# Optimization experiments

Measured on AMD Instinct MI355X. Metric: run time of the kernel, lower is better.

Reference implementation:

```python
import jax, jax.numpy as jnp
import numpy as np

N = 50000
E = 800000
NHID = 128
NOUT = 64
NLAYER = 4
BN_EPS = 1e-5


def setup_inputs() -> dict:
    key = jax.random.key(0)
    ks = jax.random.split(key, 4)
    x = jax.random.normal(ks[0], (N, NHID), dtype=jnp.float32)
    edge_index = jax.random.randint(ks[1], (2, E), 0, N, dtype=jnp.int32)
    Ws = jax.random.normal(ks[2], (NLAYER, NHID, NHID), dtype=jnp.float32) / np.sqrt(NHID)
    bs = jnp.zeros((NLAYER, NHID), dtype=jnp.float32)
    gammas = jnp.ones((NLAYER, NHID), dtype=jnp.float32)
    betas = jnp.zeros((NLAYER, NHID), dtype=jnp.float32)
    Wout = jax.random.normal(ks[3], (NHID, NOUT), dtype=jnp.float32) / np.sqrt(NHID)
    bout = jnp.zeros((NOUT,), dtype=jnp.float32)
    return {"x": x, "edge_index": edge_index, "Ws": Ws, "bs": bs,
            "gammas": gammas, "betas": betas, "Wout": Wout, "bout": bout}


def _gcn_conv(x, src, dst, norm, W, b):
    # GCNConv: h = x W, then symmetric-normalized scatter-add over edges (+ self loops already in src/dst)
    h = x @ W                                   # [N, nhid]
    msgs = h[src] * norm[:, None]               # [E+N, nhid] gather + scale
    agg = jax.ops.segment_sum(msgs, dst, num_segments=N)  # scatter-add
    return agg + b


def _batchnorm(x, gamma, beta):
    mean = jnp.mean(x, axis=0)
    var = jnp.mean(jnp.square(x - mean), axis=0)  # biased var (torch BN)
    return (x - mean) * jax.lax.rsqrt(var + BN_EPS) * gamma + beta


def reference(x, edge_index, Ws, bs, gammas, betas, Wout, bout):
    # add self loops
    loops = jnp.arange(N, dtype=edge_index.dtype)
    src = jnp.concatenate([edge_index[0], loops])
    dst = jnp.concatenate([edge_index[1], loops])
    # symmetric degree normalization: deg^-1/2[src] * deg^-1/2[dst]
    deg = jax.ops.segment_sum(jnp.ones_like(dst, dtype=x.dtype), dst, num_segments=N)
    dinv = jax.lax.rsqrt(jnp.maximum(deg, 1.0))
    norm = dinv[src] * dinv[dst]

    prev = x
    for l in range(NLAYER):
        h = _gcn_conv(x, src, dst, norm, Ws[l], bs[l])
        h = _batchnorm(h, gammas[l], betas[l])
        h = jax.nn.relu(h)
        # dropout p=0.0 -> identity
        x = h + prev  # residual
        prev = x
    return x @ Wout + bout
```

## Files before the change

### kernel.cpp

```cpp
#include <hip/hip_runtime.h>

#define NN 50000
#define NE 800000
#define NH 128
#define NO 64
#define NL 4
#define BN_EPS 1e-5f
#define NB1 ((NN + 255) / 256)

typedef __attribute__((ext_vector_type(8))) short short8;
typedef __attribute__((ext_vector_type(4))) float f32x4;

__device__ inline unsigned short f2bf(float f) {
    unsigned int u = __float_as_uint(f);
    return (unsigned short)((u + 0x7fffu + ((u >> 16) & 1u)) >> 16);
}
__device__ inline float bflo(unsigned int u) { return __uint_as_float(u << 16); }
__device__ inline float bfhi(unsigned int u) { return __uint_as_float(u & 0xffff0000u); }
__device__ inline unsigned pk(float a, float b) {
    return (unsigned)f2bf(a) | ((unsigned)f2bf(b) << 16);
}

__global__ void k_degrank(const int* __restrict__ dst, int* __restrict__ deg,
                          int* __restrict__ rank) {
    int base = (blockIdx.x * 256 + threadIdx.x) * 4;
    if (base >= NE) return;
    int4 d4 = *(const int4*)&dst[base];
    int4 r4;
    r4.x = atomicAdd(&deg[d4.x], 1);
    r4.y = atomicAdd(&deg[d4.y], 1);
    r4.z = atomicAdd(&deg[d4.z], 1);
    r4.w = atomicAdd(&deg[d4.w], 1);
    *(int4*)&rank[base] = r4;
}

__global__ void k_scan1(const int* __restrict__ deg, int* __restrict__ off,
                        int* __restrict__ aux, float* __restrict__ dinv) {
    __shared__ int ls[256];
    int i = blockIdx.x * 256 + threadIdx.x;
    int v = (i < NN) ? deg[i] : 0;
    ls[threadIdx.x] = v;
    __syncthreads();
    for (int s = 1; s < 256; s <<= 1) {
        int t = (threadIdx.x >= s) ? ls[threadIdx.x - s] : 0;
        __syncthreads();
        ls[threadIdx.x] += t;
        __syncthreads();
    }
    if (i < NN) {
        off[i] = ls[threadIdx.x] - v;
        dinv[i] = rsqrtf((float)v + 1.0f);
    }
    if (threadIdx.x == 255) aux[blockIdx.x] = ls[255];
}

__global__ void k_scan2(int* __restrict__ aux) {
    __shared__ int ls[256];
    int v = (threadIdx.x < NB1) ? aux[threadIdx.x] : 0;
    ls[threadIdx.x] = v;
    __syncthreads();
    for (int s = 1; s < 256; s <<= 1) {
        int t = (threadIdx.x >= s) ? ls[threadIdx.x - s] : 0;
        __syncthreads();
        ls[threadIdx.x] += t;
        __syncthreads();
    }
    if (threadIdx.x < NB1) aux[threadIdx.x] = ls[threadIdx.x] - v;
}

__global__ void k_scan3(int* __restrict__ off, const int* __restrict__ aux) {
    int i = blockIdx.x * 256 + threadIdx.x;
    if (i < NN) off[i] += aux[blockIdx.x];
}

__global__ void k_fill(const int* __restrict__ src, const int* __restrict__ dst,
                       const int* __restrict__ off, const int* __restrict__ rank,
                       int* __restrict__ csr) {
    int base = (blockIdx.x * 256 + threadIdx.x) * 4;
    if (base >= NE) return;
    int4 d4 = *(const int4*)&dst[base];
    int4 r4 = *(const int4*)&rank[base];
    int4 s4 = *(const int4*)&src[base];
    int o0 = off[d4.x], o1 = off[d4.y], o2 = off[d4.z], o3 = off[d4.w];
    csr[o0 + r4.x] = s4.x;
    csr[o1 + r4.y] = s4.y;
    csr[o2 + r4.z] = s4.z;
    csr[o3 + r4.w] = s4.w;
}

__global__ void k_pack(const float* __restrict__ Ws, const float* __restrict__ Wout,
                       unsigned short* __restrict__ Wpk, unsigned short* __restrict__ Wopk) {
    int t = blockIdx.x * 256 + threadIdx.x;
    if (t < NL * 16384) {
        int l = t >> 14, r = t & 16383;
        int ks = r >> 12, ct = (r >> 9) & 7, lane = (r >> 3) & 63, i = r & 7;
        int k = ks * 32 + (lane >> 4) * 8 + i;
        int n = ct * 16 + (lane & 15);
        Wpk[t] = f2bf(Ws[l * 16384 + k * 128 + n]);
    } else if (t < NL * 16384 + 8192) {
        int r = t - NL * 16384;
        int ks = r >> 11, ct = (r >> 9) & 3, lane = (r >> 3) & 63, i = r & 7;
        int k = ks * 32 + (lane >> 4) * 8 + i;
        int n = ct * 16 + (lane & 15);
        Wopk[r] = f2bf(Wout[k * 64 + n]);
    }
}

__global__ __launch_bounds__(256) void k_fg0(const float* __restrict__ X,
                                             const unsigned short* __restrict__ Wpk,
                                             const float* __restrict__ dinv,
                                             unsigned short* __restrict__ Hd) {
    int w = threadIdx.x >> 6, l = threadIdx.x & 63;
    int row0 = blockIdx.x * 64 + w * 16;
    int lo = l & 15, hi = l >> 4;
    int arow = row0 + lo;
    int crow = (arow < NN) ? arow : NN - 1;
    short8 frag[4];
#pragma unroll
    for (int g = 0; g < 4; g++) {
        int cs = g * 32 + hi * 8;
        float4 p0 = *(const float4*)&X[(size_t)crow * NH + cs];
        float4 p1 = *(const float4*)&X[(size_t)crow * NH + cs + 4];
        short8 f;
        f[0] = (short)f2bf(p0.x); f[1] = (short)f2bf(p0.y);
        f[2] = (short)f2bf(p0.z); f[3] = (short)f2bf(p0.w);
        f[4] = (short)f2bf(p1.x); f[5] = (short)f2bf(p1.y);
        f[6] = (short)f2bf(p1.z); f[7] = (short)f2bf(p1.w);
        frag[g] = f;
    }
    const short8* Wv = (const short8*)Wpk;
    int srow = row0 + hi * 4;
    float dv[4];
#pragma unroll
    for (int r = 0; r < 4; r++) dv[r] = (srow + r < NN) ? dinv[srow + r] : 0.0f;
#pragma unroll
    for (int ct = 0; ct < 8; ct++) {
        f32x4 acc = {0.0f, 0.0f, 0.0f, 0.0f};
#pragma unroll
        for (int g = 0; g < 4; g++)
            acc = __builtin_amdgcn_mfma_f32_16x16x32_bf16(frag[g], Wv[(g * 8 + ct) * 64 + l], acc, 0, 0, 0);
        int col = ct * 16 + lo;
#pragma unroll
        for (int r = 0; r < 4; r++) {
            int grow = srow + r;
            if (grow < NN) Hd[grow * NH + col] = f2bf(acc[r] * dv[r]);
        }
    }
}

__global__ __launch_bounds__(256) void k_fg(const unsigned short* __restrict__ AGGb,
                                            const float* __restrict__ scale,
                                            const float* __restrict__ shift,
                                            const float* __restrict__ Xprev,
                                            float* __restrict__ Xout,
                                            const unsigned short* __restrict__ Wpk,
                                            const float* __restrict__ dinv,
                                            unsigned short* __restrict__ Hd) {
    int w = threadIdx.x >> 6, l = threadIdx.x & 63;
    int row0 = blockIdx.x * 64 + w * 16;
    int lo = l & 15, hi = l >> 4;
    int arow = row0 + lo;
    bool valid = arow < NN;
    int crow = valid ? arow : NN - 1;
    short8 frag[4];
#pragma unroll
    for (int g = 0; g < 4; g++) {
        int cs = g * 32 + hi * 8;
        uint4 ab = *(const uint4*)&AGGb[(size_t)crow * NH + cs];
        float4 p0 = *(const float4*)&Xprev[(size_t)crow * NH + cs];
        float4 p1 = *(const float4*)&Xprev[(size_t)crow * NH + cs + 4];
        float4 sc0 = *(const float4*)&scale[cs];
        float4 sc1 = *(const float4*)&scale[cs + 4];
        float4 sh0 = *(const float4*)&shift[cs];
        float4 sh1 = *(const float4*)&shift[cs + 4];
        float o0 = fmaxf(fmaf(bflo(ab.x), sc0.x, sh0.x), 0.0f) + p0.x;
        float o1 = fmaxf(fmaf(bfhi(ab.x), sc0.y, sh0.y), 0.0f) + p0.y;
        float o2 = fmaxf(fmaf(bflo(ab.y), sc0.z, sh0.z), 0.0f) + p0.z;
        float o3 = fmaxf(fmaf(bfhi(ab.y), sc0.w, sh0.w), 0.0f) + p0.w;
        float o4 = fmaxf(fmaf(bflo(ab.z), sc1.x, sh1.x), 0.0f) + p1.x;
        float o5 = fmaxf(fmaf(bfhi(ab.z), sc1.y, sh1.y), 0.0f) + p1.y;
        float o6 = fmaxf(fmaf(bflo(ab.w), sc1.z, sh1.z), 0.0f) + p1.z;
        float o7 = fmaxf(fmaf(bfhi(ab.w), sc1.w, sh1.w), 0.0f) + p1.w;
        if (valid) {
            float4 s0 = {o0, o1, o2, o3}, s1 = {o4, o5, o6, o7};
            *(float4*)&Xout[(size_t)arow * NH + cs] = s0;
            *(float4*)&Xout[(size_t)arow * NH + cs + 4] = s1;
        }
        short8 f;
        f[0] = (short)f2bf(o0); f[1] = (short)f2bf(o1);
        f[2] = (short)f2bf(o2); f[3] = (short)f2bf(o3);
        f[4] = (short)f2bf(o4); f[5] = (short)f2bf(o5);
        f[6] = (short)f2bf(o6); f[7] = (short)f2bf(o7);
        frag[g] = f;
    }
    const short8* Wv = (const short8*)Wpk;
    int srow = row0 + hi * 4;
    float dv[4];
#pragma unroll
    for (int r = 0; r < 4; r++) dv[r] = (srow + r < NN) ? dinv[srow + r] : 0.0f;
#pragma unroll
    for (int ct = 0; ct < 8; ct++) {
        f32x4 acc = {0.0f, 0.0f, 0.0f, 0.0f};
#pragma unroll
        for (int g = 0; g < 4; g++)
            acc = __builtin_amdgcn_mfma_f32_16x16x32_bf16(frag[g], Wv[(g * 8 + ct) * 64 + l], acc, 0, 0, 0);
        int col = ct * 16 + lo;
#pragma unroll
        for (int r = 0; r < 4; r++) {
            int grow = srow + r;
            if (grow < NN) Hd[grow * NH + col] = f2bf(acc[r] * dv[r]);
        }
    }
}

__global__ __launch_bounds__(256) void k_fgout(const unsigned short* __restrict__ AGGb,
                                               const float* __restrict__ scale,
                                               const float* __restrict__ shift,
                                               const float* __restrict__ Xprev,
                                               const unsigned short* __restrict__ Wpk,
                                               const float* __restrict__ b,
                                               float* __restrict__ out) {
    int w = threadIdx.x >> 6, l = threadIdx.x & 63;
    int row0 = blockIdx.x * 64 + w * 16;
    int lo = l & 15, hi = l >> 4;
    int arow = row0 + lo;
    int crow = (arow < NN) ? arow : NN - 1;
    short8 frag[4];
#pragma unroll
    for (int g = 0; g < 4; g++) {
        int cs = g * 32 + hi * 8;
        uint4 ab = *(const uint4*)&AGGb[(size_t)crow * NH + cs];
        float4 p0 = *(const float4*)&Xprev[(size_t)crow * NH + cs];
        float4 p1 = *(const float4*)&Xprev[(size_t)crow * NH + cs + 4];
        float4 sc0 = *(const float4*)&scale[cs];
        float4 sc1 = *(const float4*)&scale[cs + 4];
        float4 sh0 = *(const float4*)&shift[cs];
        float4 sh1 = *(const float4*)&shift[cs + 4];
        short8 f;
        f[0] = (short)f2bf(fmaxf(fmaf(bflo(ab.x), sc0.x, sh0.x), 0.0f) + p0.x);
        f[1] = (short)f2bf(fmaxf(fmaf(bfhi(ab.x), sc0.y, sh0.y), 0.0f) + p0.y);
        f[2] = (short)f2bf(fmaxf(fmaf(bflo(ab.y), sc0.z, sh0.z), 0.0f) + p0.z);
        f[3] = (short)f2bf(fmaxf(fmaf(bfhi(ab.y), sc0.w, sh0.w), 0.0f) + p0.w);
        f[4] = (short)f2bf(fmaxf(fmaf(bflo(ab.z), sc1.x, sh1.x), 0.0f) + p1.x);
        f[5] = (short)f2bf(fmaxf(fmaf(bfhi(ab.z), sc1.y, sh1.y), 0.0f) + p1.y);
        f[6] = (short)f2bf(fmaxf(fmaf(bflo(ab.w), sc1.z, sh1.z), 0.0f) + p1.z);
        f[7] = (short)f2bf(fmaxf(fmaf(bfhi(ab.w), sc1.w, sh1.w), 0.0f) + p1.w);
        frag[g] = f;
    }
    const short8* Wv = (const short8*)Wpk;
    int srow = row0 + hi * 4;
#pragma unroll
    for (int ct = 0; ct < 4; ct++) {
        f32x4 acc = {0.0f, 0.0f, 0.0f, 0.0f};
#pragma unroll
        for (int g = 0; g < 4; g++)
            acc = __builtin_amdgcn_mfma_f32_16x16x32_bf16(frag[g], Wv[(g * 4 + ct) * 64 + l], acc, 0, 0, 0);
        int col = ct * 16 + lo;
        float bb = b[col];
#pragma unroll
        for (int r = 0; r < 4; r++) {
            int grow = srow + r;
            if (grow < NN) out[grow * NO + col] = acc[r] + bb;
        }
    }
}

__global__ __launch_bounds__(256) void k_gather(const unsigned short* __restrict__ Hd,
                                                const int* __restrict__ csr,
                                                const int* __restrict__ off,
                                                const int* __restrict__ deg,
                                                const float* __restrict__ dinv,
                                                unsigned short* __restrict__ AGGb) {
    int g = blockIdx.x * 16 + (threadIdx.x >> 4);
    if (g >= NN) return;
    int q = threadIdx.x & 15;
    const uint4* Hv = (const uint4*)Hd;
    int o = off[g], d = deg[g];
    uint4 h = Hv[g * 16 + q];
    float a0 = bflo(h.x), a1 = bfhi(h.x);
    float a2 = bflo(h.y), a3 = bfhi(h.y);
    float a4 = bflo(h.z), a5 = bfhi(h.z);
    float a6 = bflo(h.w), a7 = bfhi(h.w);
    int j = 0;
    for (; j + 4 <= d; j += 4) {
        int s0 = csr[o + j], s1 = csr[o + j + 1];
        int s2 = csr[o + j + 2], s3 = csr[o + j + 3];
        uint4 h0 = Hv[s0 * 16 + q];
        uint4 h1 = Hv[s1 * 16 + q];
        uint4 h2 = Hv[s2 * 16 + q];
        uint4 h3 = Hv[s3 * 16 + q];
        a0 += (bflo(h0.x) + bflo(h1.x)) + (bflo(h2.x) + bflo(h3.x));
        a1 += (bfhi(h0.x) + bfhi(h1.x)) + (bfhi(h2.x) + bfhi(h3.x));
        a2 += (bflo(h0.y) + bflo(h1.y)) + (bflo(h2.y) + bflo(h3.y));
        a3 += (bfhi(h0.y) + bfhi(h1.y)) + (bfhi(h2.y) + bfhi(h3.y));
        a4 += (bflo(h0.z) + bflo(h1.z)) + (bflo(h2.z) + bflo(h3.z));
        a5 += (bfhi(h0.z) + bfhi(h1.z)) + (bfhi(h2.z) + bfhi(h3.z));
        a6 += (bflo(h0.w) + bflo(h1.w)) + (bflo(h2.w) + bflo(h3.w));
        a7 += (bfhi(h0.w) + bfhi(h1.w)) + (bfhi(h2.w) + bfhi(h3.w));
    }
    for (; j < d; j++) {
        int s0 = csr[o + j];
        uint4 h0 = Hv[s0 * 16 + q];
        a0 += bflo(h0.x); a1 += bfhi(h0.x);
        a2 += bflo(h0.y); a3 += bfhi(h0.y);
        a4 += bflo(h0.z); a5 += bfhi(h0.z);
        a6 += bflo(h0.w); a7 += bfhi(h0.w);
    }
    float dv = dinv[g];
    uint4 u;
    u.x = pk(a0 * dv, a1 * dv);
    u.y = pk(a2 * dv, a3 * dv);
    u.z = pk(a4 * dv, a5 * dv);
    u.w = pk(a6 * dv, a7 * dv);
    ((uint4*)AGGb)[g * 16 + q] = u;
}

__global__ __launch_bounds__(256) void k_bn_stats(const unsigned short* __restrict__ AGGb,
                                                  float* __restrict__ sums,
                                                  float* __restrict__ sumsq) {
    int tid = threadIdx.x;
    int cq = tid & 31;
    int rg = tid >> 5;
    float s0 = 0, s1 = 0, s2 = 0, s3 = 0;
    float q0 = 0, q1 = 0, q2 = 0, q3 = 0;
    for (int r = blockIdx.x * 8 + rg; r < NN; r += gridDim.x * 8) {
        uint2 u = *(const uint2*)&AGGb[(size_t)r * NH + cq * 4];
        float v0 = bflo(u.x), v1 = bfhi(u.x), v2 = bflo(u.y), v3 = bfhi(u.y);
        s0 += v0; s1 += v1; s2 += v2; s3 += v3;
        q0 = fmaf(v0, v0, q0); q1 = fmaf(v1, v1, q1);
        q2 = fmaf(v2, v2, q2); q3 = fmaf(v3, v3, q3);
    }
    __shared__ float ls[256][4], lq[256][4];
    ls[tid][0] = s0; ls[tid][1] = s1; ls[tid][2] = s2; ls[tid][3] = s3;
    lq[tid][0] = q0; lq[tid][1] = q1; lq[tid][2] = q2; lq[tid][3] = q3;
    __syncthreads();
    if (rg == 0) {
        float t0 = s0, t1 = s1, t2 = s2, t3 = s3;
        float u0 = q0, u1 = q1, u2 = q2, u3 = q3;
        for (int g = 1; g < 8; g++) {
            t0 += ls[g * 32 + cq][0]; t1 += ls[g * 32 + cq][1];
            t2 += ls[g * 32 + cq][2]; t3 += ls[g * 32 + cq][3];
            u0 += lq[g * 32 + cq][0]; u1 += lq[g * 32 + cq][1];
            u2 += lq[g * 32 + cq][2]; u3 += lq[g * 32 + cq][3];
        }
        atomicAdd(&sums[cq * 4 + 0], t0); atomicAdd(&sums[cq * 4 + 1], t1);
        atomicAdd(&sums[cq * 4 + 2], t2); atomicAdd(&sums[cq * 4 + 3], t3);
        atomicAdd(&sumsq[cq * 4 + 0], u0); atomicAdd(&sumsq[cq * 4 + 1], u1);
        atomicAdd(&sumsq[cq * 4 + 2], u2); atomicAdd(&sumsq[cq * 4 + 3], u3);
    }
}

__global__ void k_bn_fin(const float* __restrict__ sums, const float* __restrict__ sumsq,
                         const float* __restrict__ gamma, const float* __restrict__ beta,
                         float* __restrict__ scale, float* __restrict__ shift) {
    int c = threadIdx.x;
    if (c < NH) {
        float mean = sums[c] * (1.0f / NN);
        float var = sumsq[c] * (1.0f / NN) - mean * mean;
        float istd = rsqrtf(var + BN_EPS);
        float sc = istd * gamma[c];
        scale[c] = sc;
        shift[c] = beta[c] - mean * sc;
    }
}

extern "C" void kernel_launch(void* const* d_in, const int* in_sizes, int n_in,
                              void* d_out, int out_size, void* d_ws, size_t ws_size,
                              hipStream_t stream) {
    const float* x    = (const float*)d_in[0];
    const int*   ei   = (const int*)d_in[1];
    const float* Ws   = (const float*)d_in[2];
    const float* gam  = (const float*)d_in[4];
    const float* bet  = (const float*)d_in[5];
    const float* Wout = (const float*)d_in[6];
    const float* bout = (const float*)d_in[7];
    float* out = (float*)d_out;

    const int* src = ei;
    const int* dst = ei + NE;

    char* p = (char*)d_ws;
    auto alloc = [&](size_t bytes) { char* r = p; p += (bytes + 255) & ~(size_t)255; return r; };
    int*   deg_i = (int*)alloc(NN * 4);
    int*   off   = (int*)alloc(NN * 4);
    int*   rank  = (int*)alloc((size_t)NE * 4);
    int*   aux   = (int*)alloc(256 * 4);
    int*   csr   = (int*)alloc((size_t)NE * 4);
    float* dinv  = (float*)alloc(NN * 4);
    float* XA    = (float*)alloc((size_t)NN * NH * 4);
    float* XB    = (float*)alloc((size_t)NN * NH * 4);
    unsigned short* Hd   = (unsigned short*)alloc((size_t)NN * NH * 2);
    unsigned short* AGGb = (unsigned short*)alloc((size_t)NN * NH * 2);
    unsigned short* Wpk  = (unsigned short*)alloc((size_t)NL * NH * NH * 2);
    unsigned short* Wopk = (unsigned short*)alloc((size_t)NH * NO * 2);
    float* stats = (float*)alloc(NL * 2 * NH * 4);
    float* scale = (float*)alloc(NH * 4);
    float* shift = (float*)alloc(NH * 4);

    hipMemsetAsync(deg_i, 0, NN * 4, stream);
    hipMemsetAsync(stats, 0, NL * 2 * NH * 4, stream);
    k_degrank<<<(NE / 4 + 255) / 256, 256, 0, stream>>>(dst, deg_i, rank);
    k_scan1<<<NB1, 256, 0, stream>>>(deg_i, off, aux, dinv);
    k_scan2<<<1, 256, 0, stream>>>(aux);
    k_scan3<<<NB1, 256, 0, stream>>>(off, aux);
    k_fill<<<(NE / 4 + 255) / 256, 256, 0, stream>>>(src, dst, off, rank, csr);
    k_pack<<<(NL * 16384 + 8192 + 255) / 256, 256, 0, stream>>>(Ws, Wout, Wpk, Wopk);

    const int GB = (NN + 63) / 64;

    k_fg0<<<GB, 256, 0, stream>>>(x, Wpk, dinv, Hd);

    const float* xprev = x;
    for (int l = 0; l < NL; l++) {
        float* sums  = stats + (size_t)l * 2 * NH;
        float* sumsq = sums + NH;
        k_gather<<<(NN + 15) / 16, 256, 0, stream>>>(Hd, csr, off, deg_i, dinv, AGGb);
        k_bn_stats<<<128, 256, 0, stream>>>(AGGb, sums, sumsq);
        k_bn_fin<<<1, 128, 0, stream>>>(sums, sumsq, gam + l * NH, bet + l * NH, scale, shift);
        if (l < NL - 1) {
            float* Xout = (l & 1) ? XB : XA;
            k_fg<<<GB, 256, 0, stream>>>(AGGb, scale, shift, xprev, Xout,
                                         Wpk + (size_t)(l + 1) * 16384, dinv, Hd);
            xprev = Xout;
        } else {
            k_fgout<<<GB, 256, 0, stream>>>(AGGb, scale, shift, xprev, Wopk, bout, out);
        }
    }
}
```

Baseline: 385.8 us.

## Fuse BN statistics into gather via per-block partials, drop scan3 kernel

The gather kernel now computes per-block column sums and sums of squares of the aggregated rows with shuffles and shared memory. It writes them to a partials buffer, and a new 128-block reduction kernel turns them into BN scale and shift. This removes the separate stats pass over AGGb, the float atomics, the finalize kernel and the stats memset. The scan3 kernel is also removed by adding the block offset from aux at each use. Degree counting now handles two edges per thread instead of four. The stats are taken from the fp32 values before bf16 rounding, which changes numerics slightly, and every gather block now pays for an extra reduction.

```diff
diff --git a/kernel.cpp b/kernel.cpp
--- a/kernel.cpp
+++ b/kernel.cpp
@@ -7,6 +7,7 @@
 #define NL 4
 #define BN_EPS 1e-5f
 #define NB1 ((NN + 255) / 256)
+#define NGB (NN / 16)
 
 typedef __attribute__((ext_vector_type(8))) short short8;
 typedef __attribute__((ext_vector_type(4))) float f32x4;
@@ -23,15 +24,13 @@
 
 __global__ void k_degrank(const int* __restrict__ dst, int* __restrict__ deg,
                           int* __restrict__ rank) {
-    int base = (blockIdx.x * 256 + threadIdx.x) * 4;
+    int base = (blockIdx.x * 256 + threadIdx.x) * 2;
     if (base >= NE) return;
-    int4 d4 = *(const int4*)&dst[base];
-    int4 r4;
-    r4.x = atomicAdd(&deg[d4.x], 1);
-    r4.y = atomicAdd(&deg[d4.y], 1);
-    r4.z = atomicAdd(&deg[d4.z], 1);
-    r4.w = atomicAdd(&deg[d4.w], 1);
-    *(int4*)&rank[base] = r4;
+    int2 d2 = *(const int2*)&dst[base];
+    int2 r2;
+    r2.x = atomicAdd(&deg[d2.x], 1);
+    r2.y = atomicAdd(&deg[d2.y], 1);
+    *(int2*)&rank[base] = r2;
 }
 
 __global__ void k_scan1(const int* __restrict__ deg, int* __restrict__ off,
@@ -68,24 +67,18 @@
     if (threadIdx.x < NB1) aux[threadIdx.x] = ls[threadIdx.x] - v;
 }
 
-__global__ void k_scan3(int* __restrict__ off, const int* __restrict__ aux) {
-    int i = blockIdx.x * 256 + threadIdx.x;
-    if (i < NN) off[i] += aux[blockIdx.x];
-}
-
 __global__ void k_fill(const int* __restrict__ src, const int* __restrict__ dst,
-                       const int* __restrict__ off, const int* __restrict__ rank,
-                       int* __restrict__ csr) {
+                       const int* __restrict__ off, const int* __restrict__ aux,
+                       const int* __restrict__ rank, int* __restrict__ csr) {
     int base = (blockIdx.x * 256 + threadIdx.x) * 4;
     if (base >= NE) return;
     int4 d4 = *(const int4*)&dst[base];
     int4 r4 = *(const int4*)&rank[base];
     int4 s4 = *(const int4*)&src[base];
-    int o0 = off[d4.x], o1 = off[d4.y], o2 = off[d4.z], o3 = off[d4.w];
-    csr[o0 + r4.x] = s4.x;
-    csr[o1 + r4.y] = s4.y;
-    csr[o2 + r4.z] = s4.z;
-    csr[o3 + r4.w] = s4.w;
+    csr[off[d4.x] + aux[d4.x >> 8] + r4.x] = s4.x;
+    csr[off[d4.y] + aux[d4.y >> 8] + r4.y] = s4.y;
+    csr[off[d4.z] + aux[d4.z >> 8] + r4.z] = s4.z;
+    csr[off[d4.w] + aux[d4.w >> 8] + r4.w] = s4.w;
 }
 
 __global__ void k_pack(const float* __restrict__ Ws, const float* __restrict__ Wout,
@@ -268,99 +261,114 @@
 __global__ __launch_bounds__(256) void k_gather(const unsigned short* __restrict__ Hd,
                                                 const int* __restrict__ csr,
                                                 const int* __restrict__ off,
+                                                const int* __restrict__ aux,
                                                 const int* __restrict__ deg,
                                                 const float* __restrict__ dinv,
-                                                unsigned short* __restrict__ AGGb) {
-    int g = blockIdx.x * 16 + (threadIdx.x >> 4);
-    if (g >= NN) return;
-    int q = threadIdx.x & 15;
-    const uint4* Hv = (const uint4*)Hd;
-    int o = off[g], d = deg[g];
-    uint4 h = Hv[g * 16 + q];
-    float a0 = bflo(h.x), a1 = bfhi(h.x);
-    float a2 = bflo(h.y), a3 = bfhi(h.y);
-    float a4 = bflo(h.z), a5 = bfhi(h.z);
-    float a6 = bflo(h.w), a7 = bfhi(h.w);
-    int j = 0;
-    for (; j + 4 <= d; j += 4) {
-        int s0 = csr[o + j], s1 = csr[o + j + 1];
-        int s2 = csr[o + j + 2], s3 = csr[o + j + 3];
-        uint4 h0 = Hv[s0 * 16 + q];
-        uint4 h1 = Hv[s1 * 16 + q];
-        uint4 h2 = Hv[s2 * 16 + q];
-        uint4 h3 = Hv[s3 * 16 + q];
-        a0 += (bflo(h0.x) + bflo(h1.x)) + (bflo(h2.x) + bflo(h3.x));
-        a1 += (bfhi(h0.x) + bfhi(h1.x)) + (bfhi(h2.x) + bfhi(h3.x));
-        a2 += (bflo(h0.y) + bflo(h1.y)) + (bflo(h2.y) + bflo(h3.y));
-        a3 += (bfhi(h0.y) + bfhi(h1.y)) + (bfhi(h2.y) + bfhi(h3.y));
-        a4 += (bflo(h0.z) + bflo(h1.z)) + (bflo(h2.z) + bflo(h3.z));
-        a5 += (bfhi(h0.z) + bfhi(h1.z)) + (bfhi(h2.z) + bfhi(h3.z));
-        a6 += (bflo(h0.w) + bflo(h1.w)) + (bflo(h2.w) + bflo(h3.w));
-        a7 += (bfhi(h0.w) + bfhi(h1.w)) + (bfhi(h2.w) + bfhi(h3.w));
-    }
-    for (; j < d; j++) {
-        int s0 = csr[o + j];
-        uint4 h0 = Hv[s0 * 16 + q];
-        a0 += bflo(h0.x); a1 += bfhi(h0.x);
-        a2 += bflo(h0.y); a3 += bfhi(h0.y);
-        a4 += bflo(h0.z); a5 += bfhi(h0.z);
-        a6 += bflo(h0.w); a7 += bfhi(h0.w);
-    }
-    float dv = dinv[g];
-    uint4 u;
-    u.x = pk(a0 * dv, a1 * dv);
-    u.y = pk(a2 * dv, a3 * dv);
-    u.z = pk(a4 * dv, a5 * dv);
-    u.w = pk(a6 * dv, a7 * dv);
-    ((uint4*)AGGb)[g * 16 + q] = u;
-}
-
-__global__ __launch_bounds__(256) void k_bn_stats(const unsigned short* __restrict__ AGGb,
-                                                  float* __restrict__ sums,
-                                                  float* __restrict__ sumsq) {
-    int tid = threadIdx.x;
-    int cq = tid & 31;
-    int rg = tid >> 5;
-    float s0 = 0, s1 = 0, s2 = 0, s3 = 0;
-    float q0 = 0, q1 = 0, q2 = 0, q3 = 0;
-    for (int r = blockIdx.x * 8 + rg; r < NN; r += gridDim.x * 8) {
-        uint2 u = *(const uint2*)&AGGb[(size_t)r * NH + cq * 4];
-        float v0 = bflo(u.x), v1 = bfhi(u.x), v2 = bflo(u.y), v3 = bfhi(u.y);
-        s0 += v0; s1 += v1; s2 += v2; s3 += v3;
-        q0 = fmaf(v0, v0, q0); q1 = fmaf(v1, v1, q1);
-        q2 = fmaf(v2, v2, q2); q3 = fmaf(v3, v3, q3);
-    }
-    __shared__ float ls[256][4], lq[256][4];
-    ls[tid][0] = s0; ls[tid][1] = s1; ls[tid][2] = s2; ls[tid][3] = s3;
-    lq[tid][0] = q0; lq[tid][1] = q1; lq[tid][2] = q2; lq[tid][3] = q3;
+                                                unsigned short* __restrict__ AGGb,
+                                                float* __restrict__ partial) {
+    int b = blockIdx.x;
+    int slot = threadIdx.x >> 4, q = threadIdx.x & 15;
+    int g = b * 16 + slot;
+    float a0 = 0, a1 = 0, a2 = 0, a3 = 0, a4 = 0, a5 = 0, a6 = 0, a7 = 0;
+    if (g < NN) {
+        const uint4* Hv = (const uint4*)Hd;
+        int o = off[g] + aux[g >> 8];
+        int d = deg[g];
+        uint4 h = Hv[g * 16 + q];
+        a0 = bflo(h.x); a1 = bfhi(h.x);
+        a2 = bflo(h.y); a3 = bfhi(h.y);
+        a4 = bflo(h.z); a5 = bfhi(h.z);
+        a6 = bflo(h.w); a7 = bfhi(h.w);
+        int j = 0;
+        for (; j + 4 <= d; j += 4) {
+            int s0 = csr[o + j], s1 = csr[o + j + 1];
+            int s2 = csr[o + j + 2], s3 = csr[o + j + 3];
+            uint4 h0 = Hv[s0 * 16 + q];
+            uint4 h1 = Hv[s1 * 16 + q];
+            uint4 h2 = Hv[s2 * 16 + q];
+            uint4 h3 = Hv[s3 * 16 + q];
+            a0 += (bflo(h0.x) + bflo(h1.x)) + (bflo(h2.x) + bflo(h3.x));
+            a1 += (bfhi(h0.x) + bfhi(h1.x)) + (bfhi(h2.x) + bfhi(h3.x));
+            a2 += (bflo(h0.y) + bflo(h1.y)) + (bflo(h2.y) + bflo(h3.y));
+            a3 += (bfhi(h0.y) + bfhi(h1.y)) + (bfhi(h2.y) + bfhi(h3.y));
+            a4 += (bflo(h0.z) + bflo(h1.z)) + (bflo(h2.z) + bflo(h3.z));
+            a5 += (bfhi(h0.z) + bfhi(h1.z)) + (bfhi(h2.z) + bfhi(h3.z));
+            a6 += (bflo(h0.w) + bflo(h1.w)) + (bflo(h2.w) + bflo(h3.w));
+            a7 += (bfhi(h0.w) + bfhi(h1.w)) + (bfhi(h2.w) + bfhi(h3.w));
+        }
+        for (; j < d; j++) {
+            int s0 = csr[o + j];
+            uint4 h0 = Hv[s0 * 16 + q];
+            a0 += bflo(h0.x); a1 += bfhi(h0.x);
+            a2 += bflo(h0.y); a3 += bfhi(h0.y);
+            a4 += bflo(h0.z); a5 += bfhi(h0.z);
+            a6 += bflo(h0.w); a7 += bfhi(h0.w);
+        }
+        float dv = dinv[g];
+        a0 *= dv; a1 *= dv; a2 *= dv; a3 *= dv;
+        a4 *= dv; a5 *= dv; a6 *= dv; a7 *= dv;
+        uint4 u;
+        u.x = pk(a0, a1); u.y = pk(a2, a3);
+        u.z = pk(a4, a5); u.w = pk(a6, a7);
+        ((uint4*)AGGb)[g * 16 + q] = u;
+    }
+    float t0 = a0 * a0, t1 = a1 * a1, t2 = a2 * a2, t3 = a3 * a3;
+    float t4 = a4 * a4, t5 = a5 * a5, t6 = a6 * a6, t7 = a7 * a7;
+#define RED(v) v += __shfl_xor(v, 16); v += __shfl_xor(v, 32);
+    RED(a0) RED(a1) RED(a2) RED(a3) RED(a4) RED(a5) RED(a6) RED(a7)
+    RED(t0) RED(t1) RED(t2) RED(t3) RED(t4) RED(t5) RED(t6) RED(t7)
+#undef RED
+    __shared__ float ws[4][16][16];
+    int wv = threadIdx.x >> 6, lane = threadIdx.x & 63;
+    if (lane < 16) {
+        ws[wv][lane][0] = a0; ws[wv][lane][1] = a1;
+        ws[wv][lane][2] = a2; ws[wv][lane][3] = a3;
+        ws[wv][lane][4] = a4; ws[wv][lane][5] = a5;
+        ws[wv][lane][6] = a6; ws[wv][lane][7] = a7;
+        ws[wv][lane][8] = t0; ws[wv][lane][9] = t1;
+        ws[wv][lane][10] = t2; ws[wv][lane][11] = t3;
+        ws[wv][lane][12] = t4; ws[wv][lane][13] = t5;
+        ws[wv][lane][14] = t6; ws[wv][lane][15] = t7;
+    }
     __syncthreads();
-    if (rg == 0) {
-        float t0 = s0, t1 = s1, t2 = s2, t3 = s3;
-        float u0 = q0, u1 = q1, u2 = q2, u3 = q3;
-        for (int g = 1; g < 8; g++) {
-            t0 += ls[g * 32 + cq][0]; t1 += ls[g * 32 + cq][1];
-            t2 += ls[g * 32 + cq][2]; t3 += ls[g * 32 + cq][3];
-            u0 += lq[g * 32 + cq][0]; u1 += lq[g * 32 + cq][1];
-            u2 += lq[g * 32 + cq][2]; u3 += lq[g * 32 + cq][3];
-        }
-        atomicAdd(&sums[cq * 4 + 0], t0); atomicAdd(&sums[cq * 4 + 1], t1);
-        atomicAdd(&sums[cq * 4 + 2], t2); atomicAdd(&sums[cq * 4 + 3], t3);
-        atomicAdd(&sumsq[cq * 4 + 0], u0); atomicAdd(&sumsq[cq * 4 + 1], u1);
-        atomicAdd(&sumsq[cq * 4 + 2], u2); atomicAdd(&sumsq[cq * 4 + 3], u3);
-    }
-}
-
-__global__ void k_bn_fin(const float* __restrict__ sums, const float* __restrict__ sumsq,
-                         const float* __restrict__ gamma, const float* __restrict__ beta,
-                         float* __restrict__ scale, float* __restrict__ shift) {
-    int c = threadIdx.x;
-    if (c < NH) {
-        float mean = sums[c] * (1.0f / NN);
-        float var = sumsq[c] * (1.0f / NN) - mean * mean;
+    if (threadIdx.x < 16) {
+        int qq = threadIdx.x;
+#pragma unroll
+        for (int k = 0; k < 8; k++) {
+            float sv = ws[0][qq][k] + ws[1][qq][k] + ws[2][qq][k] + ws[3][qq][k];
+            float qv = ws[0][qq][k + 8] + ws[1][qq][k + 8] + ws[2][qq][k + 8] + ws[3][qq][k + 8];
+            partial[(size_t)b * 256 + qq * 8 + k] = sv;
+            partial[(size_t)b * 256 + 128 + qq * 8 + k] = qv;
+        }
+    }
+}
+
+__global__ __launch_bounds__(256) void k_statred(const float* __restrict__ partial,
+                                                 const float* __restrict__ gamma,
+                                                 const float* __restrict__ beta,
+                                                 float* __restrict__ scale,
+                                                 float* __restrict__ shift) {
+    int s = blockIdx.x;
+    int t = threadIdx.x;
+    float sum = 0.0f, sq = 0.0f;
+    for (int k = t; k < NGB; k += 256) {
+        sum += partial[(size_t)k * 256 + s];
+        sq  += partial[(size_t)k * 256 + 128 + s];
+    }
+    __shared__ float ls[256], lq[256];
+    ls[t] = sum; lq[t] = sq;
+    __syncthreads();
+    for (int st = 128; st > 0; st >>= 1) {
+        if (t < st) { ls[t] += ls[t + st]; lq[t] += lq[t + st]; }
+        __syncthreads();
+    }
+    if (t == 0) {
+        float mean = ls[0] * (1.0f / NN);
+        float var = lq[0] * (1.0f / NN) - mean * mean;
         float istd = rsqrtf(var + BN_EPS);
-        float sc = istd * gamma[c];
-        scale[c] = sc;
-        shift[c] = beta[c] - mean * sc;
+        float sc = istd * gamma[s];
+        scale[s] = sc;
+        shift[s] = beta[s] - mean * sc;
     }
 }
 
@@ -393,17 +401,15 @@
     unsigned short* AGGb = (unsigned short*)alloc((size_t)NN * NH * 2);
     unsigned short* Wpk  = (unsigned short*)alloc((size_t)NL * NH * NH * 2);
     unsigned short* Wopk = (unsigned short*)alloc((size_t)NH * NO * 2);
-    float* stats = (float*)alloc(NL * 2 * NH * 4);
+    float* partial = (float*)alloc((size_t)NGB * 256 * 4);
     float* scale = (float*)alloc(NH * 4);
     float* shift = (float*)alloc(NH * 4);
 
     hipMemsetAsync(deg_i, 0, NN * 4, stream);
-    hipMemsetAsync(stats, 0, NL * 2 * NH * 4, stream);
-    k_degrank<<<(NE / 4 + 255) / 256, 256, 0, stream>>>(dst, deg_i, rank);
+    k_degrank<<<(NE / 2 + 255) / 256, 256, 0, stream>>>(dst, deg_i, rank);
     k_scan1<<<NB1, 256, 0, stream>>>(deg_i, off, aux, dinv);
     k_scan2<<<1, 256, 0, stream>>>(aux);
-    k_scan3<<<NB1, 256, 0, stream>>>(off, aux);
-    k_fill<<<(NE / 4 + 255) / 256, 256, 0, stream>>>(src, dst, off, rank, csr);
+    k_fill<<<(NE / 4 + 255) / 256, 256, 0, stream>>>(src, dst, off, aux, rank, csr);
     k_pack<<<(NL * 16384 + 8192 + 255) / 256, 256, 0, stream>>>(Ws, Wout, Wpk, Wopk);
 
     const int GB = (NN + 63) / 64;
@@ -412,11 +418,8 @@
 
     const float* xprev = x;
     for (int l = 0; l < NL; l++) {
-        float* sums  = stats + (size_t)l * 2 * NH;
-        float* sumsq = sums + NH;
-        k_gather<<<(NN + 15) / 16, 256, 0, stream>>>(Hd, csr, off, deg_i, dinv, AGGb);
-        k_bn_stats<<<128, 256, 0, stream>>>(AGGb, sums, sumsq);
-        k_bn_fin<<<1, 128, 0, stream>>>(sums, sumsq, gam + l * NH, bet + l * NH, scale, shift);
+        k_gather<<<NGB, 256, 0, stream>>>(Hd, csr, off, aux, deg_i, dinv, AGGb, partial);
+        k_statred<<<128, 256, 0, stream>>>(partial, gam + l * NH, bet + l * NH, scale, shift);
         if (l < NL - 1) {
             float* Xout = (l & 1) ? XB : XA;
             k_fg<<<GB, 256, 0, stream>>>(AGGb, scale, shift, xprev, Xout,
```

Result: faster. 320.4 us (-16.9%).
